# Performance work log

Measured on AMD Instinct MI355X. Metric: run time of the kernel, lower is better.

The kernel has to match this reference:

```python
import jax, jax.numpy as jnp
import numpy as np

N_NODES = 100000
N_EDGES = 1600000
IN_F = 256
OUT_F = 128


def setup_inputs() -> dict:
    key = jax.random.key(0)
    k1, k2, k3, k4, k5, k6 = jax.random.split(key, 6)
    x = jax.random.normal(k1, (N_NODES, IN_F), dtype=jnp.float32)
    edge_row = jax.random.randint(k2, (N_EDGES,), 0, N_NODES)  # destination (output row)
    edge_col = jax.random.randint(k3, (N_EDGES,), 0, N_NODES)  # source (gathered node)
    edge_val = jax.random.uniform(k4, (N_EDGES,), dtype=jnp.float32)  # normalized adj weights
    # Xavier-uniform init like nn.init.xavier_uniform_
    limit = float(np.sqrt(6.0 / (IN_F + OUT_F)))
    weight = jax.random.uniform(k5, (IN_F, OUT_F), dtype=jnp.float32, minval=-limit, maxval=limit)
    bias = jnp.zeros((OUT_F,), dtype=jnp.float32)
    return {"x": x, "edge_row": edge_row, "edge_col": edge_col,
            "edge_val": edge_val, "weight": weight, "bias": bias}


def reference(x, edge_row, edge_col, edge_val, weight, bias):
    # Dense transform: h = x @ W + b   -> [N, OUT_F]
    h = x @ weight + bias
    # Sparse adjacency matmul: out[i] = sum_{e: row[e]==i} val[e] * h[col[e]]
    msg = h[edge_col] * edge_val[:, None]  # [E, OUT_F] gather + scale
    out = jax.ops.segment_sum(msg, edge_row, num_segments=N_NODES)
    return out
```

## Files before the change

kernel.cpp:

```cpp
#include <hip/hip_runtime.h>

#define IN_F 256
#define OUT_F 128
#define CAP 5120
#define EPB 4096

typedef __attribute__((ext_vector_type(8))) short short8;
typedef __attribute__((ext_vector_type(4))) float floatx4;

__device__ __forceinline__ unsigned short f2bf(float f) {
    union { float f; unsigned int u; } v; v.f = f;
    unsigned int u = v.u;
    unsigned int r = (u + 0x7FFFu + ((u >> 16) & 1u)) >> 16;
    return (unsigned short)r;
}

__global__ __launch_bounds__(256) void prep_kernel(
    const float* __restrict__ w, unsigned short* __restrict__ w_t,
    int* __restrict__ cursor, int nb)
{
    const int g = blockIdx.x * 256 + threadIdx.x;
    if (g < IN_F * OUT_F) {
        const int n = g >> 8;
        const int k = g & 255;
        w_t[n * 256 + k] = f2bf(w[k * OUT_F + n]);
    }
    const int z = g - IN_F * OUT_F;
    if (z >= 0 && z < nb) cursor[z] = 0;
}

#define XS2 264
#define HS2 136
#define GEMM_SMEM 33792

__device__ __forceinline__ void gemm_body(
    char* smem,
    const float* __restrict__ x, const unsigned short* __restrict__ w_t,
    const float* __restrict__ bias, unsigned short* __restrict__ h_bf,
    int tile, int M)
{
    unsigned short* xs = (unsigned short*)smem;

    const int tid  = threadIdx.x;
    const int w    = tid >> 6;
    const int l    = tid & 63;
    const int m16  = l & 15;
    const int g    = l >> 4;
    const int row0 = tile * 64;

    short8 bf[2][8];
    #pragma unroll
    for (int nt = 0; nt < 2; nt++)
        #pragma unroll
        for (int ks = 0; ks < 8; ks++)
            bf[nt][ks] = *(const short8*)(
                w_t + (w * 32 + nt * 16 + m16) * 256 + ks * 32 + g * 8);

    #pragma unroll
    for (int s = 0; s < 16; s++) {
        const int idx = tid + s * 256;
        const int row = idx >> 6;
        const int c4  = idx & 63;
        const int gr  = row0 + row;
        float4 v = make_float4(0.f, 0.f, 0.f, 0.f);
        if (gr < M) v = *(const float4*)(x + (size_t)gr * IN_F + c4 * 4);
        ushort4 b;
        b.x = f2bf(v.x); b.y = f2bf(v.y); b.z = f2bf(v.z); b.w = f2bf(v.w);
        *(ushort4*)(xs + row * XS2 + c4 * 4) = b;
    }
    __syncthreads();

    floatx4 acc[4][2];
    #pragma unroll
    for (int mt = 0; mt < 4; mt++) {
        acc[mt][0] = (floatx4){0.f, 0.f, 0.f, 0.f};
        acc[mt][1] = (floatx4){0.f, 0.f, 0.f, 0.f};
    }

    #pragma unroll
    for (int ks = 0; ks < 8; ks++) {
        #pragma unroll
        for (int mt = 0; mt < 4; mt++) {
            const short8 a = *(const short8*)(xs + (mt * 16 + m16) * XS2 + ks * 32 + g * 8);
            acc[mt][0] = __builtin_amdgcn_mfma_f32_16x16x32_bf16(a, bf[0][ks], acc[mt][0], 0, 0, 0);
            acc[mt][1] = __builtin_amdgcn_mfma_f32_16x16x32_bf16(a, bf[1][ks], acc[mt][1], 0, 0, 0);
        }
    }
    __syncthreads();

    unsigned short* hs = xs;
    #pragma unroll
    for (int nt = 0; nt < 2; nt++) {
        const int col = w * 32 + nt * 16 + m16;
        const float bv = bias[col];
        #pragma unroll
        for (int mt = 0; mt < 4; mt++)
            #pragma unroll
            for (int r = 0; r < 4; r++)
                hs[(mt * 16 + g * 4 + r) * HS2 + col] = f2bf(acc[mt][nt][r] + bv);
    }
    __syncthreads();

    {
        const int row = tid >> 2;
        const int seg = tid & 3;
        const int gr  = row0 + row;
        if (gr < M) {
            #pragma unroll
            for (int q = 0; q < 4; q++) {
                const uint4 v = *(const uint4*)(hs + row * HS2 + seg * 32 + q * 8);
                *(uint4*)(h_bf + (size_t)gr * OUT_F + seg * 32 + q * 8) = v;
            }
        }
    }
}

__device__ __forceinline__ void sort_body(
    char* smem, const int* __restrict__ erow, const int* __restrict__ ecol,
    const float* __restrict__ eval, int* __restrict__ cursor,
    uint2* __restrict__ tmp, int E, int nb, int blk)
{
    int* lcnt  = (int*)smem;
    int* lbase = lcnt + 512;
    for (int i = threadIdx.x; i < nb; i += 256) lcnt[i] = 0;
    __syncthreads();
    const int base = blk * EPB;
    #pragma unroll
    for (int i = 0; i < EPB / 256; i++) {
        const int e = base + i * 256 + threadIdx.x;
        if (e < E) atomicAdd(&lcnt[erow[e] >> 8], 1);
    }
    __syncthreads();
    for (int i = threadIdx.x; i < nb; i += 256) {
        const int c = lcnt[i];
        lbase[i] = c ? atomicAdd(&cursor[i], c) : 0;
        lcnt[i] = 0;
    }
    __syncthreads();
    #pragma unroll
    for (int i = 0; i < EPB / 256; i++) {
        const int e = base + i * 256 + threadIdx.x;
        if (e < E) {
            const int r = erow[e];
            const int b = r >> 8;
            const int lp = atomicAdd(&lcnt[b], 1);
            const int pos = lbase[b] + lp;
            if (pos < CAP)
                tmp[(size_t)b * CAP + pos] = make_uint2(
                    ((unsigned int)(r & 255) << 24) | (unsigned int)ecol[e],
                    __float_as_uint(eval[e]));
        }
    }
}

__device__ __forceinline__ void csr_body(
    char* smem, uint2* __restrict__ tmp, const int* __restrict__ cursor,
    int* __restrict__ start, int* __restrict__ endx, int M, int blk)
{
    int* nh   = (int*)smem;
    int* nst  = nh + 256;
    int* ncur = nst + 256;
    unsigned int* lcv = (unsigned int*)(smem + 3072);

    const int b  = blk;
    const size_t tb = (size_t)b * CAP;
    const int cnt = min(cursor[b], CAP);
    const int t  = threadIdx.x;

    nh[t] = 0;
    __syncthreads();
    for (int i = t; i < cnt; i += 256) atomicAdd(&nh[tmp[tb + i].x >> 24], 1);
    __syncthreads();

    const int v = nh[t];
    nst[t] = v;
    __syncthreads();
    for (int off = 1; off < 256; off <<= 1) {
        const int u = (t >= off) ? nst[t - off] : 0;
        __syncthreads();
        nst[t] += u;
        __syncthreads();
    }
    const int ex = nst[t] - v;
    const int node = b * 256 + t;
    const int cvbase = b * CAP * 2;
    if (node < M) { start[node] = cvbase + ex; endx[node] = cvbase + ex + v; }
    ncur[t] = ex;
    __syncthreads();

    for (int i = t; i < cnt; i += 256) {
        const uint2 p = tmp[tb + i];
        const int d  = p.x >> 24;
        const int lp = atomicAdd(&ncur[d], 1);
        const float f = __uint_as_float(p.y);
        const int q = min((int)(f * 32768.0f), 32767);
        lcv[lp] = ((p.x & 0x00FFFFFFu) << 15) | (unsigned int)q;
    }
    __syncthreads();

    unsigned int* cvp = (unsigned int*)tmp;
    for (int i = t; i < cnt; i += 256) cvp[(size_t)cvbase + i] = lcv[i];
}

__global__ __launch_bounds__(256) void k_sort_gemm(
    const int* __restrict__ erow, const int* __restrict__ ecol,
    const float* __restrict__ eval, int* __restrict__ cursor,
    uint2* __restrict__ tmp, int E, int nb, int EB,
    const float* __restrict__ x, const unsigned short* __restrict__ w_t,
    const float* __restrict__ bias, unsigned short* __restrict__ h_bf,
    int M, int tile0)
{
    __shared__ __align__(16) char smem[GEMM_SMEM];
    if ((int)blockIdx.x < EB)
        sort_body(smem, erow, ecol, eval, cursor, tmp, E, nb, blockIdx.x);
    else
        gemm_body(smem, x, w_t, bias, h_bf, tile0 + (int)blockIdx.x - EB, M);
}

__global__ __launch_bounds__(256) void k_csr_gemm(
    uint2* __restrict__ tmp, const int* __restrict__ cursor,
    int* __restrict__ start, int* __restrict__ endx, int nb,
    const float* __restrict__ x, const unsigned short* __restrict__ w_t,
    const float* __restrict__ bias, unsigned short* __restrict__ h_bf,
    int M, int tile0)
{
    __shared__ __align__(16) char smem[GEMM_SMEM];
    if ((int)blockIdx.x < nb)
        csr_body(smem, tmp, cursor, start, endx, M, blockIdx.x);
    else
        gemm_body(smem, x, w_t, bias, h_bf, tile0 + (int)blockIdx.x - nb, M);
}

__global__ __launch_bounds__(256) void gather_kernel(
    const unsigned short* __restrict__ h_bf, const int* __restrict__ start,
    const int* __restrict__ endx, const unsigned int* __restrict__ cv,
    float* __restrict__ out, int N)
{
    const int node = (blockIdx.x * 256 + threadIdx.x) >> 6;
    const int lane = threadIdx.x & 63;
    if (node >= N) return;

    const int s   = start[node];
    const int end = endx[node];
    const unsigned int* hp = (const unsigned int*)h_bf;

    float acc0 = 0.f, acc1 = 0.f;
    int j = s;
    for (; j + 8 <= end; j += 8) {
        unsigned int mu[8];
        const unsigned int* rp[8];
        #pragma unroll
        for (int u = 0; u < 8; u++) {
            mu[u] = __builtin_amdgcn_readfirstlane(cv[j + u]);
            rp[u] = hp + (size_t)(mu[u] >> 15) * 64;
        }
        unsigned int p[8];
        #pragma unroll
        for (int u = 0; u < 8; u++) p[u] = rp[u][lane];
        #pragma unroll
        for (int u = 0; u < 8; u++) {
            const float v = (float)(mu[u] & 0x7FFFu) * (1.0f / 32768.0f) + (0.5f / 32768.0f);
            acc0 += v * __uint_as_float(p[u] << 16);
            acc1 += v * __uint_as_float(p[u] & 0xFFFF0000u);
        }
    }
    for (; j < end; j++) {
        const unsigned int mu = __builtin_amdgcn_readfirstlane(cv[j]);
        const unsigned int p = *(hp + (size_t)(mu >> 15) * 64 + lane);
        const float v = (float)(mu & 0x7FFFu) * (1.0f / 32768.0f) + (0.5f / 32768.0f);
        acc0 += v * __uint_as_float(p << 16);
        acc1 += v * __uint_as_float(p & 0xFFFF0000u);
    }
    float2 o; o.x = acc0; o.y = acc1;
    *(float2*)(out + (size_t)node * OUT_F + lane * 2) = o;
}

extern "C" void kernel_launch(void* const* d_in, const int* in_sizes, int n_in,
                              void* d_out, int out_size, void* d_ws, size_t ws_size,
                              hipStream_t stream) {
    const float* x     = (const float*)d_in[0];
    const int*   erow  = (const int*)d_in[1];
    const int*   ecol  = (const int*)d_in[2];
    const float* eval  = (const float*)d_in[3];
    const float* wgt   = (const float*)d_in[4];
    const float* bias  = (const float*)d_in[5];
    float*       out   = (float*)d_out;

    const int M  = in_sizes[0] / IN_F;
    const int E  = in_sizes[1];
    const int nb = (M + 255) >> 8;
    const int EB = (E + EPB - 1) / EPB;
    const int GT = (M + 63) / 64;
    const int S1 = (GT * 45) / 100;
    const int S2 = GT - S1;

    char* ws = (char*)d_ws;
    unsigned short* h_bf = (unsigned short*)ws;  ws += (size_t)M * OUT_F * 2;
    unsigned short* w_t  = (unsigned short*)ws;  ws += (size_t)IN_F * OUT_F * 2;
    int* cursor      = (int*)ws;                 ws += ((size_t)nb * 4 + 15) & ~15ull;
    int* start       = (int*)ws;                 ws += ((size_t)M * 4 + 15) & ~15ull;
    int* endx        = (int*)ws;                 ws += ((size_t)M * 4 + 15) & ~15ull;
    uint2* tmp       = (uint2*)ws;               ws += (size_t)nb * CAP * 8;
    unsigned int* cv = (unsigned int*)tmp;

    prep_kernel<<<(IN_F * OUT_F + nb + 255) / 256, 256, 0, stream>>>(wgt, w_t, cursor, nb);

    k_sort_gemm<<<EB + S1, 256, 0, stream>>>(erow, ecol, eval, cursor, tmp, E, nb, EB,
                                             x, w_t, bias, h_bf, M, 0);

    k_csr_gemm<<<nb + S2, 256, 0, stream>>>(tmp, cursor, start, endx, nb,
                                            x, w_t, bias, h_bf, M, S1);

    const long long work = (long long)M * 64;
    gather_kernel<<<(int)((work + 255) / 256), 256, 0, stream>>>(
        h_bf, start, endx, cv, out, M);
}
```

Baseline: 306.4 us.

## Fuse CSR build with gather using ticket-ordered blocks and per-bucket flags

```diff
diff --git a/kernel.cpp b/kernel.cpp
--- a/kernel.cpp
+++ b/kernel.cpp
@@ -3,7 +3,7 @@
 #define IN_F 256
 #define OUT_F 128
 #define CAP 5120
-#define EPB 4096
+#define EPB 8192
 
 typedef __attribute__((ext_vector_type(8))) short short8;
 typedef __attribute__((ext_vector_type(4))) float floatx4;
@@ -17,7 +17,8 @@
 
 __global__ __launch_bounds__(256) void prep_kernel(
     const float* __restrict__ w, unsigned short* __restrict__ w_t,
-    int* __restrict__ cursor, int nb)
+    int* __restrict__ cursor, int* __restrict__ flag,
+    int* __restrict__ ticket, int nb)
 {
     const int g = blockIdx.x * 256 + threadIdx.x;
     if (g < IN_F * OUT_F) {
@@ -25,8 +26,8 @@
         const int k = g & 255;
         w_t[n * 256 + k] = f2bf(w[k * OUT_F + n]);
     }
-    const int z = g - IN_F * OUT_F;
-    if (z >= 0 && z < nb) cursor[z] = 0;
+    if (g < nb) { cursor[g] = 0; flag[g] = 0; }
+    if (g == 0) ticket[0] = 0;
 }
 
 #define XS2 264
@@ -125,7 +126,6 @@
     for (int i = threadIdx.x; i < nb; i += 256) lcnt[i] = 0;
     __syncthreads();
     const int base = blk * EPB;
-    #pragma unroll
     for (int i = 0; i < EPB / 256; i++) {
         const int e = base + i * 256 + threadIdx.x;
         if (e < E) atomicAdd(&lcnt[erow[e] >> 8], 1);
@@ -137,7 +137,6 @@
         lcnt[i] = 0;
     }
     __syncthreads();
-    #pragma unroll
     for (int i = 0; i < EPB / 256; i++) {
         const int e = base + i * 256 + threadIdx.x;
         if (e < E) {
@@ -207,41 +206,57 @@
     const float* __restrict__ eval, int* __restrict__ cursor,
     uint2* __restrict__ tmp, int E, int nb, int EB,
     const float* __restrict__ x, const unsigned short* __restrict__ w_t,
-    const float* __restrict__ bias, unsigned short* __restrict__ h_bf,
-    int M, int tile0)
+    const float* __restrict__ bias, unsigned short* __restrict__ h_bf, int M)
 {
     __shared__ __align__(16) char smem[GEMM_SMEM];
     if ((int)blockIdx.x < EB)
         sort_body(smem, erow, ecol, eval, cursor, tmp, E, nb, blockIdx.x);
     else
-        gemm_body(smem, x, w_t, bias, h_bf, tile0 + (int)blockIdx.x - EB, M);
-}
-
-__global__ __launch_bounds__(256) void k_csr_gemm(
+        gemm_body(smem, x, w_t, bias, h_bf, (int)blockIdx.x - EB, M);
+}
+
+#define CG_SMEM 23552
+
+__global__ __launch_bounds__(256) void k_csr_gather(
     uint2* __restrict__ tmp, const int* __restrict__ cursor,
     int* __restrict__ start, int* __restrict__ endx, int nb,
-    const float* __restrict__ x, const unsigned short* __restrict__ w_t,
-    const float* __restrict__ bias, unsigned short* __restrict__ h_bf,
-    int M, int tile0)
-{
-    __shared__ __align__(16) char smem[GEMM_SMEM];
-    if ((int)blockIdx.x < nb)
-        csr_body(smem, tmp, cursor, start, endx, M, blockIdx.x);
-    else
-        gemm_body(smem, x, w_t, bias, h_bf, tile0 + (int)blockIdx.x - nb, M);
-}
-
-__global__ __launch_bounds__(256) void gather_kernel(
-    const unsigned short* __restrict__ h_bf, const int* __restrict__ start,
-    const int* __restrict__ endx, const unsigned int* __restrict__ cv,
-    float* __restrict__ out, int N)
-{
-    const int node = (blockIdx.x * 256 + threadIdx.x) >> 6;
+    int* __restrict__ ticket, int* __restrict__ flag,
+    const unsigned short* __restrict__ h_bf, float* __restrict__ out, int M)
+{
+    __shared__ __align__(16) char smem[CG_SMEM];
+    __shared__ int task_s;
+    if (threadIdx.x == 0) task_s = atomicAdd(ticket, 1);
+    __syncthreads();
+    const int task = task_s;
+
+    if (task < nb) {
+        csr_body(smem, tmp, cursor, start, endx, M, task);
+        __syncthreads();
+        if (threadIdx.x == 0) {
+            __threadfence();
+            __hip_atomic_store(&flag[task], 1, __ATOMIC_RELEASE,
+                               __HIP_MEMORY_SCOPE_AGENT);
+        }
+        return;
+    }
+
+    const int grp = task - nb;
+    if (grp * 4 >= M) return;
+    const int b = grp >> 6;
+    if (threadIdx.x == 0) {
+        while (__hip_atomic_load(&flag[b], __ATOMIC_ACQUIRE,
+                                 __HIP_MEMORY_SCOPE_AGENT) == 0)
+            __builtin_amdgcn_s_sleep(16);
+    }
+    __syncthreads();
+
+    const int node = grp * 4 + (threadIdx.x >> 6);
     const int lane = threadIdx.x & 63;
-    if (node >= N) return;
+    if (node >= M) return;
 
     const int s   = start[node];
     const int end = endx[node];
+    const unsigned int* cv = (const unsigned int*)tmp;
     const unsigned int* hp = (const unsigned int*)h_bf;
 
     float acc0 = 0.f, acc1 = 0.f;
@@ -291,27 +306,24 @@
     const int nb = (M + 255) >> 8;
     const int EB = (E + EPB - 1) / EPB;
     const int GT = (M + 63) / 64;
-    const int S1 = (GT * 45) / 100;
-    const int S2 = GT - S1;
+    const int NG = (M + 3) / 4;
 
     char* ws = (char*)d_ws;
     unsigned short* h_bf = (unsigned short*)ws;  ws += (size_t)M * OUT_F * 2;
     unsigned short* w_t  = (unsigned short*)ws;  ws += (size_t)IN_F * OUT_F * 2;
     int* cursor      = (int*)ws;                 ws += ((size_t)nb * 4 + 15) & ~15ull;
+    int* flag        = (int*)ws;                 ws += ((size_t)nb * 4 + 15) & ~15ull;
+    int* ticket      = (int*)ws;                 ws += 16;
     int* start       = (int*)ws;                 ws += ((size_t)M * 4 + 15) & ~15ull;
     int* endx        = (int*)ws;                 ws += ((size_t)M * 4 + 15) & ~15ull;
     uint2* tmp       = (uint2*)ws;               ws += (size_t)nb * CAP * 8;
-    unsigned int* cv = (unsigned int*)tmp;
-
-    prep_kernel<<<(IN_F * OUT_F + nb + 255) / 256, 256, 0, stream>>>(wgt, w_t, cursor, nb);
-
-    k_sort_gemm<<<EB + S1, 256, 0, stream>>>(erow, ecol, eval, cursor, tmp, E, nb, EB,
-                                             x, w_t, bias, h_bf, M, 0);
-
-    k_csr_gemm<<<nb + S2, 256, 0, stream>>>(tmp, cursor, start, endx, nb,
-                                            x, w_t, bias, h_bf, M, S1);
-
-    const long long work = (long long)M * 64;
-    gather_kernel<<<(int)((work + 255) / 256), 256, 0, stream>>>(
-        h_bf, start, endx, cv, out, M);
-}
+
+    prep_kernel<<<(IN_F * OUT_F + 255) / 256, 256, 0, stream>>>(
+        wgt, w_t, cursor, flag, ticket, nb);
+
+    k_sort_gemm<<<EB + GT, 256, 0, stream>>>(erow, ecol, eval, cursor, tmp, E, nb, EB,
+                                             x, w_t, bias, h_bf, M);
+
+    k_csr_gather<<<nb + NG, 256, 0, stream>>>(tmp, cursor, start, endx, nb,
+                                              ticket, flag, h_bf, out, M);
+}
```

After: 761.4 us. 2.48x slower.
